# Performance work log

Hardware: AMD Instinct MI355X
Metric: run time of the kernel (lower is better)

The kernel has to match this reference:

```python
import jax, jax.numpy as jnp
import numpy as np

# Finite-difference stencils along a given axis with one-sided boundary handling:
#  'f' : forward diff  d[i]=(X[i+1]-X[i])/h, last voxel copies previous diff
#  'b' : backward diff d[i]=(X[i]-X[i-1])/h, first voxel copies next diff
#  'c' : central diff  d[i]=(X[i+1]-X[i-1])/(2h), one-sided at boundaries

def _g(X, axis, h, kind):
    Xm = jnp.moveaxis(X, axis, 0)
    d = (Xm[1:] - Xm[:-1]) / h  # length n-1 one-step diffs
    if kind == 'f':
        r = jnp.concatenate([d, d[-1:]], axis=0)
    elif kind == 'b':
        r = jnp.concatenate([d[:1], d], axis=0)
    else:  # central
        r = jnp.concatenate([d[:1], (Xm[2:] - Xm[:-2]) / (2.0 * h), d[-1:]], axis=0)
    return jnp.moveaxis(r, 0, axis)

HX = HY = HZ = 1.0  # data_spacing = [1,1,1]

dXc = lambda X: _g(X, 1, HX, 'c')
dYc = lambda X: _g(X, 2, HY, 'c')
dZc = lambda X: _g(X, 3, HZ, 'c')
dXf = lambda X: _g(X, 1, HX, 'f')
dYf = lambda X: _g(X, 2, HY, 'f')
dZf = lambda X: _g(X, 3, HZ, 'f')
dXb = lambda X: _g(X, 1, HX, 'b')
dYb = lambda X: _g(X, 2, HY, 'b')
dZb = lambda X: _g(X, 3, HZ, 'b')


def setup_inputs() -> dict:
    key = jax.random.key(0)
    ks = jax.random.split(key, 10)
    shp = (2, 160, 160, 160)
    f32 = jnp.float32
    return {
        'C':   jax.random.normal(ks[0], shp, f32),
        'Vx':  jax.random.normal(ks[1], shp, f32),
        'Vy':  jax.random.normal(ks[2], shp, f32),
        'Vz':  jax.random.normal(ks[3], shp, f32),
        'Dxx': jax.random.uniform(ks[4], shp, f32),
        'Dxy': jax.random.normal(ks[5], shp, f32) * 0.1,
        'Dxz': jax.random.normal(ks[6], shp, f32) * 0.1,
        'Dyy': jax.random.uniform(ks[7], shp, f32),
        'Dyz': jax.random.normal(ks[8], shp, f32) * 0.1,
        'Dzz': jax.random.uniform(ks[9], shp, f32),
    }


def reference(C, Vx, Vy, Vz, Dxx, Dxy, Dxz, Dyy, Dyz, Dzz):
    # --- diffusion term: Grad_fullD (3D, full symmetric tensor D) ---
    Cx_c, Cy_c, Cz_c = dXc(C), dYc(C), dZc(C)        # central grads of C
    Cx_f, Cy_f, Cz_f = dXf(C), dYf(C), dZf(C)        # forward grads of C
    diff = ((dXc(Dxx) + dYc(Dxy) + dZc(Dxz)) * Cx_c
            + (dXc(Dxy) + dYc(Dyy) + dZc(Dyz)) * Cy_c
            + (dXc(Dxz) + dYc(Dyz) + dZc(Dzz)) * Cz_c
            + Dxx * dXb(Cx_f) + Dyy * dYb(Cy_f) + Dzz * dZb(Cz_f)
            + Dxy * (dXb(Cy_f) + dYb(Cx_f))
            + Dyz * (dYb(Cz_f) + dZb(Cy_f))
            + Dxz * (dZb(Cx_f) + dXb(Cz_f)))
    # --- advection term: Grad_vectorV (upwind per-voxel on sign of V) ---
    C_x = jnp.where(Vx > 0, dXb(C), dXf(C))
    C_y = jnp.where(Vy > 0, dYb(C), dYf(C))
    C_z = jnp.where(Vz > 0, dZb(C), dZf(C))
    adv = -(Vx * C_x + Vy * C_y + Vz * C_z) - C * (dXc(Vx) + dYc(Vy) + dZc(Vz))
    return diff + adv
```

## Files before the change

### kernel.cpp

```cpp
#include <hip/hip_runtime.h>

#define N   160
#define SX  (N * N)
#define SY  N

__global__ __launch_bounds__(640) void piano_energy_kernel(
    const float* __restrict__ C,   const float* __restrict__ Vx,
    const float* __restrict__ Vy,  const float* __restrict__ Vz,
    const float* __restrict__ Dxx, const float* __restrict__ Dxy,
    const float* __restrict__ Dxz, const float* __restrict__ Dyy,
    const float* __restrict__ Dyz, const float* __restrict__ Dzz,
    float* __restrict__ out)
{
    const int z = threadIdx.x;
    const int y = blockIdx.x * 4 + threadIdx.y;
    const int x = blockIdx.y;
    const int b = blockIdx.z;

    const int idx = ((b * N + x) * N + y) * N + z;

    const bool xlo = (x > 0), xhi = (x < N - 1);
    const bool ylo = (y > 0), yhi = (y < N - 1);
    const bool zlo = (z > 0), zhi = (z < N - 1);

    const int oxp = xhi ?  SX : 0,  oxm = xlo ? -SX : 0;
    const int oyp = yhi ?  SY : 0,  oym = ylo ? -SY : 0;
    const int ozp = zhi ?   1 : 0,  ozm = zlo ?  -1 : 0;

    const float sx = (xlo && xhi) ? 0.5f : 1.f;
    const float sy = (ylo && yhi) ? 0.5f : 1.f;
    const float sz = (zlo && zhi) ? 0.5f : 1.f;

    const float c0  = C[idx];
    const float cxp = C[idx + oxp], cxm = C[idx + oxm];
    const float cyp = C[idx + oyp], cym = C[idx + oym];
    const float czp = C[idx + ozp], czm = C[idx + ozm];

    const float Cx_c = sx * (cxp - cxm);
    const float Cy_c = sy * (cyp - cym);
    const float Cz_c = sz * (czp - czm);
    const float Cx_f = xhi ? (cxp - c0) : (c0 - cxm);
    const float Cy_f = yhi ? (cyp - c0) : (c0 - cym);
    const float Cz_f = zhi ? (czp - c0) : (c0 - czm);
    const float Cx_b = xlo ? (c0 - cxm) : (cxp - c0);
    const float Cy_b = ylo ? (c0 - cym) : (cyp - c0);
    const float Cz_b = zlo ? (c0 - czm) : (czp - c0);

    float sXX, sYY, sZZ;
    if (!xhi)      sXX = 0.f;
    else if (xlo)  sXX = cxp - 2.f * c0 + cxm;
    else           sXX = C[idx + 2 * SX] - 2.f * cxp + c0;
    if (!yhi)      sYY = 0.f;
    else if (ylo)  sYY = cyp - 2.f * c0 + cym;
    else           sYY = C[idx + 2 * SY] - 2.f * cyp + c0;
    if (!zhi)      sZZ = 0.f;
    else if (zlo)  sZZ = czp - 2.f * c0 + czm;
    else           sZZ = C[idx + 2] - 2.f * czp + c0;

    const int obx1 = xlo ? 0 : SX,  obx0 = obx1 - SX;
    const int oby1 = ylo ? 0 : SY,  oby0 = oby1 - SY;
    const int obz1 = zlo ? 0 : 1,   obz0 = obz1 - 1;
    const int ofx0 = xhi ? 0 : -SX;
    const int ofy0 = yhi ? 0 : -SY;
    const int ofz0 = zhi ? 0 : -1;

    float cXY;
    if (xlo && xhi && ylo && yhi) {
        cXY = cxp + cxm + cyp + cym - 2.f * c0
            - C[idx - SX + SY] - C[idx + SX - SY];
    } else {
        cXY = (C[idx + obx1 + oyp] - C[idx + obx1 + ofy0])
            - (C[idx + obx0 + oyp] - C[idx + obx0 + ofy0])
            + (C[idx + oby1 + oxp] - C[idx + oby1 + ofx0])
            - (C[idx + oby0 + oxp] - C[idx + oby0 + ofx0]);
    }

    float cXZ;
    if (xlo && xhi && zlo && zhi) {
        cXZ = cxp + cxm + czp + czm - 2.f * c0
            - C[idx + SX - 1] - C[idx - SX + 1];
    } else {
        cXZ = (C[idx + obz1 + oxp] - C[idx + obz1 + ofx0])
            - (C[idx + obz0 + oxp] - C[idx + obz0 + ofx0])
            + (C[idx + obx1 + ozp] - C[idx + obx1 + ofz0])
            - (C[idx + obx0 + ozp] - C[idx + obx0 + ofz0]);
    }

    float cYZ;
    if (ylo && yhi && zlo && zhi) {
        cYZ = cyp + cym + czp + czm - 2.f * c0
            - C[idx + SY - 1] - C[idx - SY + 1];
    } else {
        cYZ = (C[idx + obz1 + oyp] - C[idx + obz1 + ofy0])
            - (C[idx + obz0 + oyp] - C[idx + obz0 + ofy0])
            + (C[idx + oby1 + ozp] - C[idx + oby1 + ofz0])
            - (C[idx + oby0 + ozp] - C[idx + oby0 + ofz0]);
    }

    const float dDxx_x = sx * (Dxx[idx + oxp] - Dxx[idx + oxm]);
    const float dDxy_x = sx * (Dxy[idx + oxp] - Dxy[idx + oxm]);
    const float dDxy_y = sy * (Dxy[idx + oyp] - Dxy[idx + oym]);
    const float dDxz_x = sx * (Dxz[idx + oxp] - Dxz[idx + oxm]);
    const float dDxz_z = sz * (Dxz[idx + ozp] - Dxz[idx + ozm]);
    const float dDyy_y = sy * (Dyy[idx + oyp] - Dyy[idx + oym]);
    const float dDyz_y = sy * (Dyz[idx + oyp] - Dyz[idx + oym]);
    const float dDyz_z = sz * (Dyz[idx + ozp] - Dyz[idx + ozm]);
    const float dDzz_z = sz * (Dzz[idx + ozp] - Dzz[idx + ozm]);

    const float t1 = dDxx_x + dDxy_y + dDxz_z;
    const float t2 = dDxy_x + dDyy_y + dDyz_z;
    const float t3 = dDxz_x + dDyz_y + dDzz_z;

    const float Dxx0 = Dxx[idx], Dyy0 = Dyy[idx], Dzz0 = Dzz[idx];
    const float Dxy0 = Dxy[idx], Dyz0 = Dyz[idx], Dxz0 = Dxz[idx];

    const float diff = t1 * Cx_c + t2 * Cy_c + t3 * Cz_c
                     + Dxx0 * sXX + Dyy0 * sYY + Dzz0 * sZZ
                     + Dxy0 * cXY + Dyz0 * cYZ + Dxz0 * cXZ;

    const float Vx0 = Vx[idx], Vy0 = Vy[idx], Vz0 = Vz[idx];
    const float dVx = sx * (Vx[idx + oxp] - Vx[idx + oxm]);
    const float dVy = sy * (Vy[idx + oyp] - Vy[idx + oym]);
    const float dVz = sz * (Vz[idx + ozp] - Vz[idx + ozm]);

    const float C_x = (Vx0 > 0.f) ? Cx_b : Cx_f;
    const float C_y = (Vy0 > 0.f) ? Cy_b : Cy_f;
    const float C_z = (Vz0 > 0.f) ? Cz_b : Cz_f;

    const float adv = -(Vx0 * C_x + Vy0 * C_y + Vz0 * C_z)
                    - c0 * (dVx + dVy + dVz);

    out[idx] = diff + adv;
}

extern "C" void kernel_launch(void* const* d_in, const int* in_sizes, int n_in,
                              void* d_out, int out_size, void* d_ws, size_t ws_size,
                              hipStream_t stream) {
    const float* C   = (const float*)d_in[0];
    const float* Vx  = (const float*)d_in[1];
    const float* Vy  = (const float*)d_in[2];
    const float* Vz  = (const float*)d_in[3];
    const float* Dxx = (const float*)d_in[4];
    const float* Dxy = (const float*)d_in[5];
    const float* Dxz = (const float*)d_in[6];
    const float* Dyy = (const float*)d_in[7];
    const float* Dyz = (const float*)d_in[8];
    const float* Dzz = (const float*)d_in[9];
    float* out = (float*)d_out;

    dim3 grid(N / 4, N, 2);
    dim3 block(N, 4, 1);
    hipLaunchKernelGGL(piano_energy_kernel, grid, block, 0, stream,
                       C, Vx, Vy, Vz, Dxx, Dxy, Dxz, Dyy, Dyz, Dzz, out);
}
```

Measured before the change: 357.6 us.

## Vectorize stencil to four z-points per thread with float4 loads and swizzled block mapping

Each thread now computes four consecutive z voxels, loading neighbour rows as float4 and reusing them in registers for the z-direction stencils. This cuts redundant per-voxel scalar loads and per-element address arithmetic. The grid is flattened with a block-index swizzle that interleaves x slices, meant to improve L2 locality across concurrently running blocks. Launch bounds change to 320 threads with a minimum occupancy hint. Register pressure rises, and the boundary paths still fall back to scalar gathers.

```diff
diff --git a/kernel.cpp b/kernel.cpp
--- a/kernel.cpp
+++ b/kernel.cpp
@@ -4,7 +4,27 @@
 #define SX  (N * N)
 #define SY  N
 
-__global__ __launch_bounds__(640) void piano_energy_kernel(
+
+struct R4 { float a[4]; };
+struct R6 { float a[6]; };
+
+__device__ __forceinline__ R4 ld4(const float* __restrict__ p, int row, int z0) {
+    const float4 m = *reinterpret_cast<const float4*>(p + row * N + z0);
+    R4 r; r.a[0] = m.x; r.a[1] = m.y; r.a[2] = m.z; r.a[3] = m.w;
+    return r;
+}
+
+__device__ __forceinline__ R6 ld6(const float* __restrict__ p, int row, int z0,
+                                  int zL, int zR) {
+    const float4 m = *reinterpret_cast<const float4*>(p + row * N + z0);
+    R6 r;
+    r.a[0] = p[row * N + z0 + zL];
+    r.a[1] = m.x; r.a[2] = m.y; r.a[3] = m.z; r.a[4] = m.w;
+    r.a[5] = p[row * N + z0 + zR];
+    return r;
+}
+
+__global__ __launch_bounds__(320, 4) void piano_energy_kernel(
     const float* __restrict__ C,   const float* __restrict__ Vx,
     const float* __restrict__ Vy,  const float* __restrict__ Vz,
     const float* __restrict__ Dxx, const float* __restrict__ Dxy,
@@ -12,125 +32,250 @@
     const float* __restrict__ Dyz, const float* __restrict__ Dzz,
     float* __restrict__ out)
 {
-    const int z = threadIdx.x;
-    const int y = blockIdx.x * 4 + threadIdx.y;
-    const int x = blockIdx.y;
-    const int b = blockIdx.z;
-
-    const int idx = ((b * N + x) * N + y) * N + z;
+    const int tz = threadIdx.x;
+    const int z0 = tz << 2;
+
+    const int id = blockIdx.x;
+    const int w  = (id & 7) * 800 + (id >> 3);
+    const int x  = w % N;
+    const int g  = w / N;
+    const int y  = (g % 20) * 8 + threadIdx.y;
+    const int b  = g / 20;
+
+    const int r0  = (b * N + x) * N + y;
+    const int idx = r0 * N + z0;
 
     const bool xlo = (x > 0), xhi = (x < N - 1);
     const bool ylo = (y > 0), yhi = (y < N - 1);
-    const bool zlo = (z > 0), zhi = (z < N - 1);
-
-    const int oxp = xhi ?  SX : 0,  oxm = xlo ? -SX : 0;
-    const int oyp = yhi ?  SY : 0,  oym = ylo ? -SY : 0;
-    const int ozp = zhi ?   1 : 0,  ozm = zlo ?  -1 : 0;
+    const bool zlo0 = (tz > 0), zhi3 = (tz < 39);
+
+    const int oxp_r = xhi ?  N : 0, oxm_r = xlo ? -N : 0;
+    const int oyp_r = yhi ?  1 : 0, oym_r = ylo ? -1 : 0;
+    const int zL = zlo0 ? -1 : 0;
+    const int zR = zhi3 ?  4 : 3;
 
     const float sx = (xlo && xhi) ? 0.5f : 1.f;
     const float sy = (ylo && yhi) ? 0.5f : 1.f;
-    const float sz = (zlo && zhi) ? 0.5f : 1.f;
-
-    const float c0  = C[idx];
-    const float cxp = C[idx + oxp], cxm = C[idx + oxm];
-    const float cyp = C[idx + oyp], cym = C[idx + oym];
-    const float czp = C[idx + ozp], czm = C[idx + ozm];
-
-    const float Cx_c = sx * (cxp - cxm);
-    const float Cy_c = sy * (cyp - cym);
-    const float Cz_c = sz * (czp - czm);
-    const float Cx_f = xhi ? (cxp - c0) : (c0 - cxm);
-    const float Cy_f = yhi ? (cyp - c0) : (c0 - cym);
-    const float Cz_f = zhi ? (czp - c0) : (c0 - czm);
-    const float Cx_b = xlo ? (c0 - cxm) : (cxp - c0);
-    const float Cy_b = ylo ? (c0 - cym) : (cyp - c0);
-    const float Cz_b = zlo ? (c0 - czm) : (czp - c0);
-
-    float sXX, sYY, sZZ;
-    if (!xhi)      sXX = 0.f;
-    else if (xlo)  sXX = cxp - 2.f * c0 + cxm;
-    else           sXX = C[idx + 2 * SX] - 2.f * cxp + c0;
-    if (!yhi)      sYY = 0.f;
-    else if (ylo)  sYY = cyp - 2.f * c0 + cym;
-    else           sYY = C[idx + 2 * SY] - 2.f * cyp + c0;
-    if (!zhi)      sZZ = 0.f;
-    else if (zlo)  sZZ = czp - 2.f * c0 + czm;
-    else           sZZ = C[idx + 2] - 2.f * czp + c0;
-
-    const int obx1 = xlo ? 0 : SX,  obx0 = obx1 - SX;
-    const int oby1 = ylo ? 0 : SY,  oby0 = oby1 - SY;
-    const int obz1 = zlo ? 0 : 1,   obz0 = obz1 - 1;
-    const int ofx0 = xhi ? 0 : -SX;
-    const int ofy0 = yhi ? 0 : -SY;
-    const int ofz0 = zhi ? 0 : -1;
-
-    float cXY;
-    if (xlo && xhi && ylo && yhi) {
-        cXY = cxp + cxm + cyp + cym - 2.f * c0
-            - C[idx - SX + SY] - C[idx + SX - SY];
-    } else {
-        cXY = (C[idx + obx1 + oyp] - C[idx + obx1 + ofy0])
-            - (C[idx + obx0 + oyp] - C[idx + obx0 + ofy0])
-            + (C[idx + oby1 + oxp] - C[idx + oby1 + ofx0])
-            - (C[idx + oby0 + oxp] - C[idx + oby0 + ofx0]);
-    }
-
-    float cXZ;
-    if (xlo && xhi && zlo && zhi) {
-        cXZ = cxp + cxm + czp + czm - 2.f * c0
-            - C[idx + SX - 1] - C[idx - SX + 1];
-    } else {
-        cXZ = (C[idx + obz1 + oxp] - C[idx + obz1 + ofx0])
-            - (C[idx + obz0 + oxp] - C[idx + obz0 + ofx0])
-            + (C[idx + obx1 + ozp] - C[idx + obx1 + ofz0])
-            - (C[idx + obx0 + ozp] - C[idx + obx0 + ofz0]);
-    }
-
-    float cYZ;
-    if (ylo && yhi && zlo && zhi) {
-        cYZ = cyp + cym + czp + czm - 2.f * c0
-            - C[idx + SY - 1] - C[idx - SY + 1];
-    } else {
-        cYZ = (C[idx + obz1 + oyp] - C[idx + obz1 + ofy0])
-            - (C[idx + obz0 + oyp] - C[idx + obz0 + ofy0])
-            + (C[idx + oby1 + ozp] - C[idx + oby1 + ofz0])
-            - (C[idx + oby0 + ozp] - C[idx + oby0 + ofz0]);
-    }
-
-    const float dDxx_x = sx * (Dxx[idx + oxp] - Dxx[idx + oxm]);
-    const float dDxy_x = sx * (Dxy[idx + oxp] - Dxy[idx + oxm]);
-    const float dDxy_y = sy * (Dxy[idx + oyp] - Dxy[idx + oym]);
-    const float dDxz_x = sx * (Dxz[idx + oxp] - Dxz[idx + oxm]);
-    const float dDxz_z = sz * (Dxz[idx + ozp] - Dxz[idx + ozm]);
-    const float dDyy_y = sy * (Dyy[idx + oyp] - Dyy[idx + oym]);
-    const float dDyz_y = sy * (Dyz[idx + oyp] - Dyz[idx + oym]);
-    const float dDyz_z = sz * (Dyz[idx + ozp] - Dyz[idx + ozm]);
-    const float dDzz_z = sz * (Dzz[idx + ozp] - Dzz[idx + ozm]);
-
-    const float t1 = dDxx_x + dDxy_y + dDxz_z;
-    const float t2 = dDxy_x + dDyy_y + dDyz_z;
-    const float t3 = dDxz_x + dDyz_y + dDzz_z;
-
-    const float Dxx0 = Dxx[idx], Dyy0 = Dyy[idx], Dzz0 = Dzz[idx];
-    const float Dxy0 = Dxy[idx], Dyz0 = Dyz[idx], Dxz0 = Dxz[idx];
-
-    const float diff = t1 * Cx_c + t2 * Cy_c + t3 * Cz_c
-                     + Dxx0 * sXX + Dyy0 * sYY + Dzz0 * sZZ
-                     + Dxy0 * cXY + Dyz0 * cYZ + Dxz0 * cXZ;
-
-    const float Vx0 = Vx[idx], Vy0 = Vy[idx], Vz0 = Vz[idx];
-    const float dVx = sx * (Vx[idx + oxp] - Vx[idx + oxm]);
-    const float dVy = sy * (Vy[idx + oyp] - Vy[idx + oym]);
-    const float dVz = sz * (Vz[idx + ozp] - Vz[idx + ozm]);
-
-    const float C_x = (Vx0 > 0.f) ? Cx_b : Cx_f;
-    const float C_y = (Vy0 > 0.f) ? Cy_b : Cy_f;
-    const float C_z = (Vz0 > 0.f) ? Cz_b : Cz_f;
-
-    const float adv = -(Vx0 * C_x + Vy0 * C_y + Vz0 * C_z)
-                    - c0 * (dVx + dVy + dVz);
-
-    out[idx] = diff + adv;
+
+    const int oxp = xhi ? SX : 0, ofx0 = xhi ? 0 : -SX;
+    const int oyp = yhi ? SY : 0, ofy0 = yhi ? 0 : -SY;
+    const int obx1 = xlo ? 0 : SX, obx0 = obx1 - SX;
+    const int oby1 = ylo ? 0 : SY, oby0 = oby1 - SY;
+
+    const R6 Cc  = ld6(C, r0,         z0, zL, zR);
+    const R6 Cxp = ld6(C, r0 + oxp_r, z0, zL, zR);
+    const R6 Cxm = ld6(C, r0 + oxm_r, z0, zL, zR);
+    const R6 Cyp = ld6(C, r0 + oyp_r, z0, zL, zR);
+    const R6 Cym = ld6(C, r0 + oym_r, z0, zL, zR);
+    const R4 Ca  = ld4(C, r0 + oxm_r + oyp_r, z0);
+    const R4 Cb  = ld4(C, r0 + oxp_r + oym_r, z0);
+
+    R4 Cx2 = {}; R4 Cy2 = {};
+    if (!xlo && xhi) Cx2 = ld4(C, r0 + 2 * N, z0);
+    if (!ylo && yhi) Cy2 = ld4(C, r0 + 2, z0);
+
+    float Cxc[4], Cyc[4], Czc[4];
+    float sXXa[4], sYYa[4], sZZa[4], cXYa[4], cXZa[4], cYZa[4];
+
+#pragma unroll
+    for (int e = 0; e < 4; ++e) {
+        const bool zlo = (e > 0) || zlo0;
+        const bool zhi = (e < 3) || zhi3;
+        const float sz = (zlo && zhi) ? 0.5f : 1.f;
+        const float c0  = Cc.a[e + 1];
+        const float cxp = Cxp.a[e + 1], cxm = Cxm.a[e + 1];
+        const float cyp = Cyp.a[e + 1], cym = Cym.a[e + 1];
+        const float czp = zhi ? Cc.a[e + 2] : c0;
+        const float czm = zlo ? Cc.a[e]     : c0;
+
+        Cxc[e] = sx * (cxp - cxm);
+        Cyc[e] = sy * (cyp - cym);
+        Czc[e] = sz * (czp - czm);
+
+        float sXX, sYY, sZZ;
+        if (!xhi)      sXX = 0.f;
+        else if (xlo)  sXX = cxp - 2.f * c0 + cxm;
+        else           sXX = Cx2.a[e] - 2.f * cxp + c0;
+        if (!yhi)      sYY = 0.f;
+        else if (ylo)  sYY = cyp - 2.f * c0 + cym;
+        else           sYY = Cy2.a[e] - 2.f * cyp + c0;
+        if (!zhi)      sZZ = 0.f;
+        else if (zlo)  sZZ = czp - 2.f * c0 + czm;
+        else           sZZ = Cc.a[(e + 3 > 5) ? 5 : e + 3] - 2.f * czp + c0;
+        sXXa[e] = sXX; sYYa[e] = sYY; sZZa[e] = sZZ;
+
+        const int gi = idx + e;
+        if (xlo && xhi && ylo && yhi) {
+            cXYa[e] = cxp + cxm + cyp + cym - 2.f * c0 - Ca.a[e] - Cb.a[e];
+        } else {
+            cXYa[e] = (C[gi + obx1 + oyp] - C[gi + obx1 + ofy0])
+                    - (C[gi + obx0 + oyp] - C[gi + obx0 + ofy0])
+                    + (C[gi + oby1 + oxp] - C[gi + oby1 + ofx0])
+                    - (C[gi + oby0 + oxp] - C[gi + oby0 + ofx0]);
+        }
+        if (xlo && xhi && zlo && zhi) {
+            cXZa[e] = cxp + cxm + czp + czm - 2.f * c0
+                    - Cxp.a[e] - Cxm.a[e + 2];
+        } else {
+            const int ozp = zhi ? 1 : 0;
+            const int obz1 = zlo ? 0 : 1, obz0 = obz1 - 1;
+            const int ofz0 = zhi ? 0 : -1;
+            cXZa[e] = (C[gi + obz1 + oxp] - C[gi + obz1 + ofx0])
+                    - (C[gi + obz0 + oxp] - C[gi + obz0 + ofx0])
+                    + (C[gi + obx1 + ozp] - C[gi + obx1 + ofz0])
+                    - (C[gi + obx0 + ozp] - C[gi + obx0 + ofz0]);
+        }
+        if (ylo && yhi && zlo && zhi) {
+            cYZa[e] = cyp + cym + czp + czm - 2.f * c0
+                    - Cyp.a[e] - Cym.a[e + 2];
+        } else {
+            const int ozp = zhi ? 1 : 0;
+            const int obz1 = zlo ? 0 : 1, obz0 = obz1 - 1;
+            const int ofz0 = zhi ? 0 : -1;
+            cYZa[e] = (C[gi + obz1 + oyp] - C[gi + obz1 + ofy0])
+                    - (C[gi + obz0 + oyp] - C[gi + obz0 + ofy0])
+                    + (C[gi + oby1 + ozp] - C[gi + oby1 + ofz0])
+                    - (C[gi + oby0 + ozp] - C[gi + oby0 + ofz0]);
+        }
+    }
+
+    float t1a[4], t2a[4], t3a[4], acc[4];
+
+    {
+        const R4 c = ld4(Dxx, r0, z0);
+        const R4 p = ld4(Dxx, r0 + oxp_r, z0);
+        const R4 m = ld4(Dxx, r0 + oxm_r, z0);
+#pragma unroll
+        for (int e = 0; e < 4; ++e) {
+            t1a[e] = sx * (p.a[e] - m.a[e]);
+            acc[e] = c.a[e] * sXXa[e];
+        }
+    }
+    {
+        const R4 c  = ld4(Dxy, r0, z0);
+        const R4 xp = ld4(Dxy, r0 + oxp_r, z0);
+        const R4 xm = ld4(Dxy, r0 + oxm_r, z0);
+        const R4 yp = ld4(Dxy, r0 + oyp_r, z0);
+        const R4 ym = ld4(Dxy, r0 + oym_r, z0);
+#pragma unroll
+        for (int e = 0; e < 4; ++e) {
+            t1a[e] += sy * (yp.a[e] - ym.a[e]);
+            t2a[e]  = sx * (xp.a[e] - xm.a[e]);
+            acc[e] += c.a[e] * cXYa[e];
+        }
+    }
+    {
+        const R6 c  = ld6(Dxz, r0, z0, zL, zR);
+        const R4 xp = ld4(Dxz, r0 + oxp_r, z0);
+        const R4 xm = ld4(Dxz, r0 + oxm_r, z0);
+#pragma unroll
+        for (int e = 0; e < 4; ++e) {
+            const bool zlo = (e > 0) || zlo0;
+            const bool zhi = (e < 3) || zhi3;
+            const float sz = (zlo && zhi) ? 0.5f : 1.f;
+            const float zpv = zhi ? c.a[e + 2] : c.a[e + 1];
+            const float zmv = zlo ? c.a[e]     : c.a[e + 1];
+            t1a[e] += sz * (zpv - zmv);
+            t3a[e]  = sx * (xp.a[e] - xm.a[e]);
+            acc[e] += c.a[e + 1] * cXZa[e];
+        }
+    }
+    {
+        const R4 c  = ld4(Dyy, r0, z0);
+        const R4 yp = ld4(Dyy, r0 + oyp_r, z0);
+        const R4 ym = ld4(Dyy, r0 + oym_r, z0);
+#pragma unroll
+        for (int e = 0; e < 4; ++e) {
+            t2a[e] += sy * (yp.a[e] - ym.a[e]);
+            acc[e] += c.a[e] * sYYa[e];
+        }
+    }
+    {
+        const R6 c  = ld6(Dyz, r0, z0, zL, zR);
+        const R4 yp = ld4(Dyz, r0 + oyp_r, z0);
+        const R4 ym = ld4(Dyz, r0 + oym_r, z0);
+#pragma unroll
+        for (int e = 0; e < 4; ++e) {
+            const bool zlo = (e > 0) || zlo0;
+            const bool zhi = (e < 3) || zhi3;
+            const float sz = (zlo && zhi) ? 0.5f : 1.f;
+            const float zpv = zhi ? c.a[e + 2] : c.a[e + 1];
+            const float zmv = zlo ? c.a[e]     : c.a[e + 1];
+            t2a[e] += sz * (zpv - zmv);
+            t3a[e] += sy * (yp.a[e] - ym.a[e]);
+            acc[e] += c.a[e + 1] * cYZa[e];
+        }
+    }
+    {
+        const R6 c = ld6(Dzz, r0, z0, zL, zR);
+#pragma unroll
+        for (int e = 0; e < 4; ++e) {
+            const bool zlo = (e > 0) || zlo0;
+            const bool zhi = (e < 3) || zhi3;
+            const float sz = (zlo && zhi) ? 0.5f : 1.f;
+            const float zpv = zhi ? c.a[e + 2] : c.a[e + 1];
+            const float zmv = zlo ? c.a[e]     : c.a[e + 1];
+            t3a[e] += sz * (zpv - zmv);
+            acc[e] += c.a[e + 1] * sZZa[e];
+        }
+    }
+
+#pragma unroll
+    for (int e = 0; e < 4; ++e)
+        acc[e] += t1a[e] * Cxc[e] + t2a[e] * Cyc[e] + t3a[e] * Czc[e];
+
+    {
+        const R4 c = ld4(Vx, r0, z0);
+        const R4 p = ld4(Vx, r0 + oxp_r, z0);
+        const R4 m = ld4(Vx, r0 + oxm_r, z0);
+#pragma unroll
+        for (int e = 0; e < 4; ++e) {
+            const float c0  = Cc.a[e + 1];
+            const float cxp = Cxp.a[e + 1], cxm = Cxm.a[e + 1];
+            const float Cx_f = xhi ? (cxp - c0) : (c0 - cxm);
+            const float Cx_b = xlo ? (c0 - cxm) : (cxp - c0);
+            const float v = c.a[e];
+            acc[e] -= v * ((v > 0.f) ? Cx_b : Cx_f)
+                    + c0 * (sx * (p.a[e] - m.a[e]));
+        }
+    }
+    {
+        const R4 c = ld4(Vy, r0, z0);
+        const R4 p = ld4(Vy, r0 + oyp_r, z0);
+        const R4 m = ld4(Vy, r0 + oym_r, z0);
+#pragma unroll
+        for (int e = 0; e < 4; ++e) {
+            const float c0  = Cc.a[e + 1];
+            const float cyp = Cyp.a[e + 1], cym = Cym.a[e + 1];
+            const float Cy_f = yhi ? (cyp - c0) : (c0 - cym);
+            const float Cy_b = ylo ? (c0 - cym) : (cyp - c0);
+            const float v = c.a[e];
+            acc[e] -= v * ((v > 0.f) ? Cy_b : Cy_f)
+                    + c0 * (sy * (p.a[e] - m.a[e]));
+        }
+    }
+    {
+        const R6 c = ld6(Vz, r0, z0, zL, zR);
+#pragma unroll
+        for (int e = 0; e < 4; ++e) {
+            const bool zlo = (e > 0) || zlo0;
+            const bool zhi = (e < 3) || zhi3;
+            const float sz = (zlo && zhi) ? 0.5f : 1.f;
+            const float c0  = Cc.a[e + 1];
+            const float czp = zhi ? Cc.a[e + 2] : c0;
+            const float czm = zlo ? Cc.a[e]     : c0;
+            const float Cz_f = zhi ? (czp - c0) : (c0 - czm);
+            const float Cz_b = zlo ? (c0 - czm) : (czp - c0);
+            const float v = c.a[e + 1];
+            const float dVz = sz * ((zhi ? c.a[e + 2] : c.a[e + 1])
+                                  - (zlo ? c.a[e]     : c.a[e + 1]));
+            acc[e] -= v * ((v > 0.f) ? Cz_b : Cz_f) + c0 * dVz;
+        }
+    }
+
+    float4 o;
+    o.x = acc[0]; o.y = acc[1]; o.z = acc[2]; o.w = acc[3];
+    *reinterpret_cast<float4*>(out + idx) = o;
 }
 
 extern "C" void kernel_launch(void* const* d_in, const int* in_sizes, int n_in,
@@ -148,8 +293,8 @@
     const float* Dzz = (const float*)d_in[9];
     float* out = (float*)d_out;
 
-    dim3 grid(N / 4, N, 2);
-    dim3 block(N, 4, 1);
+    dim3 grid(6400, 1, 1);
+    dim3 block(40, 8, 1);
     hipLaunchKernelGGL(piano_energy_kernel, grid, block, 0, stream,
                        C, Vx, Vy, Vz, Dxx, Dxy, Dxz, Dyy, Dyz, Dzz, out);
 }
```

New measurement: 716.7 us. 100% more time.

## Stage stencil input tiles into LDS and swizzle block ordering

Applied to the files above, without the earlier changes.

Each block cooperatively loads the needed x-planes and y-halo rows of all ten input fields into shared memory with vectorized float4 loads, then computes the stencil from LDS. The grid is flattened and block indices are swizzled so neighbouring work is spread across the device. This aims to cut redundant global/cache reads of neighbour values, at the cost of large LDS use per block (lower occupancy) and extra reloading of x-neighbour planes across blocks.

```diff
diff --git a/kernel.cpp b/kernel.cpp
--- a/kernel.cpp
+++ b/kernel.cpp
@@ -1,10 +1,31 @@
 #include <hip/hip_runtime.h>
 
-#define N   160
-#define SX  (N * N)
-#define SY  N
-
-__global__ __launch_bounds__(640) void piano_energy_kernel(
+#define N    160
+#define SX   (N * N)
+#define SY   N
+#define ROW  160
+
+
+template<int P, int R, bool HALO>
+__device__ __forceinline__ void stage(float* __restrict__ lds, int dstRow,
+                                      const float* __restrict__ src,
+                                      int b, int x, int y0, int tid)
+{
+    const int tot = P * R * 40;
+    for (int u = tid; u < tot; u += 640) {
+        const int c = u % 40;
+        const int r = (u / 40) % R;
+        const int p = u / (40 * R);
+        const int px = (P == 3) ? min(max(x + p - 1, 0), N - 1) : x;
+        int gy = HALO ? (y0 + r - 1) : (y0 + r);
+        if (HALO) gy = min(max(gy, 0), N - 1);
+        const float4 v = *reinterpret_cast<const float4*>(
+            src + ((b * N + px) * N + gy) * N + (c << 2));
+        *reinterpret_cast<float4*>(lds + (dstRow + p * R + r) * ROW + (c << 2)) = v;
+    }
+}
+
+__global__ __launch_bounds__(640, 2) void piano_energy_kernel(
     const float* __restrict__ C,   const float* __restrict__ Vx,
     const float* __restrict__ Vy,  const float* __restrict__ Vz,
     const float* __restrict__ Dxx, const float* __restrict__ Dxy,
@@ -12,10 +33,32 @@
     const float* __restrict__ Dyz, const float* __restrict__ Dzz,
     float* __restrict__ out)
 {
-    const int z = threadIdx.x;
-    const int y = blockIdx.x * 4 + threadIdx.y;
-    const int x = blockIdx.y;
-    const int b = blockIdx.z;
+    __shared__ float lds[98 * ROW];
+
+    const int id = blockIdx.x;
+    const int w  = (id & 7) * 1600 + (id >> 3);
+    const int x  = w % N;
+    const int g  = w / N;
+    const int y0 = (g % 40) * 4;
+    const int b  = g / 40;
+
+    const int z   = threadIdx.x;
+    const int ty  = threadIdx.y;
+    const int tid = ty * 160 + z;
+    const int y   = y0 + ty;
+    const int jc  = ty + 1;
+
+    stage<3, 6, true >(lds,  0, C,   b, x, y0, tid);
+    stage<3, 4, false>(lds, 18, Dxx, b, x, y0, tid);
+    stage<3, 6, true >(lds, 30, Dxy, b, x, y0, tid);
+    stage<3, 4, false>(lds, 48, Dxz, b, x, y0, tid);
+    stage<3, 4, false>(lds, 60, Vx,  b, x, y0, tid);
+    stage<1, 6, true >(lds, 72, Dyy, b, x, y0, tid);
+    stage<1, 6, true >(lds, 78, Dyz, b, x, y0, tid);
+    stage<1, 6, true >(lds, 84, Vy,  b, x, y0, tid);
+    stage<1, 4, false>(lds, 90, Dzz, b, x, y0, tid);
+    stage<1, 4, false>(lds, 94, Vz,  b, x, y0, tid);
+    __syncthreads();
 
     const int idx = ((b * N + x) * N + y) * N + z;
 
@@ -23,18 +66,29 @@
     const bool ylo = (y > 0), yhi = (y < N - 1);
     const bool zlo = (z > 0), zhi = (z < N - 1);
 
-    const int oxp = xhi ?  SX : 0,  oxm = xlo ? -SX : 0;
-    const int oyp = yhi ?  SY : 0,  oym = ylo ? -SY : 0;
-    const int ozp = zhi ?   1 : 0,  ozm = zlo ?  -1 : 0;
+    const int xp = 1 + (xhi ? 1 : 0), xm = 1 - (xlo ? 1 : 0);
+    const int yp = jc + (yhi ? 1 : 0), ym = jc - (ylo ? 1 : 0);
+    const int zp = z + (zhi ? 1 : 0),  zm = z - (zlo ? 1 : 0);
 
     const float sx = (xlo && xhi) ? 0.5f : 1.f;
     const float sy = (ylo && yhi) ? 0.5f : 1.f;
     const float sz = (zlo && zhi) ? 0.5f : 1.f;
 
-    const float c0  = C[idx];
-    const float cxp = C[idx + oxp], cxm = C[idx + oxm];
-    const float cyp = C[idx + oyp], cym = C[idx + oym];
-    const float czp = C[idx + ozp], czm = C[idx + ozm];
+#define CL(p,j,zz)   lds[((p) * 6 + (j)) * ROW + (zz)]
+#define DXXL(p,zz)   lds[(18 + (p) * 4 + ty) * ROW + (zz)]
+#define DXYL(p,j,zz) lds[(30 + (p) * 6 + (j)) * ROW + (zz)]
+#define DXZL(p,zz)   lds[(48 + (p) * 4 + ty) * ROW + (zz)]
+#define VXL(p,zz)    lds[(60 + (p) * 4 + ty) * ROW + (zz)]
+#define DYYL(j,zz)   lds[(72 + (j)) * ROW + (zz)]
+#define DYZL(j,zz)   lds[(78 + (j)) * ROW + (zz)]
+#define VYL(j,zz)    lds[(84 + (j)) * ROW + (zz)]
+#define DZZL(zz)     lds[(90 + ty) * ROW + (zz)]
+#define VZL(zz)      lds[(94 + ty) * ROW + (zz)]
+
+    const float c0  = CL(1, jc, z);
+    const float cxp = CL(xp, jc, z), cxm = CL(xm, jc, z);
+    const float cyp = CL(1, yp, z),  cym = CL(1, ym, z);
+    const float czp = CL(1, jc, zp), czm = CL(1, jc, zm);
 
     const float Cx_c = sx * (cxp - cxm);
     const float Cy_c = sy * (cyp - cym);
@@ -52,76 +106,76 @@
     else           sXX = C[idx + 2 * SX] - 2.f * cxp + c0;
     if (!yhi)      sYY = 0.f;
     else if (ylo)  sYY = cyp - 2.f * c0 + cym;
-    else           sYY = C[idx + 2 * SY] - 2.f * cyp + c0;
+    else           sYY = CL(1, jc + 2, z) - 2.f * cyp + c0;
     if (!zhi)      sZZ = 0.f;
     else if (zlo)  sZZ = czp - 2.f * c0 + czm;
-    else           sZZ = C[idx + 2] - 2.f * czp + c0;
-
-    const int obx1 = xlo ? 0 : SX,  obx0 = obx1 - SX;
-    const int oby1 = ylo ? 0 : SY,  oby0 = oby1 - SY;
-    const int obz1 = zlo ? 0 : 1,   obz0 = obz1 - 1;
-    const int ofx0 = xhi ? 0 : -SX;
-    const int ofy0 = yhi ? 0 : -SY;
+    else           sZZ = CL(1, jc, 2) - 2.f * czp + c0;
+
+    const int obx1 = xlo ? 0 : 1, obx0 = obx1 - 1;
+    const int oby1 = ylo ? 0 : 1, oby0 = oby1 - 1;
+    const int obz1 = zlo ? 0 : 1, obz0 = obz1 - 1;
+    const int ofx0 = xhi ? 0 : -1;
+    const int ofy0 = yhi ? 0 : -1;
     const int ofz0 = zhi ? 0 : -1;
 
     float cXY;
     if (xlo && xhi && ylo && yhi) {
         cXY = cxp + cxm + cyp + cym - 2.f * c0
-            - C[idx - SX + SY] - C[idx + SX - SY];
+            - CL(0, jc + 1, z) - CL(2, jc - 1, z);
     } else {
-        cXY = (C[idx + obx1 + oyp] - C[idx + obx1 + ofy0])
-            - (C[idx + obx0 + oyp] - C[idx + obx0 + ofy0])
-            + (C[idx + oby1 + oxp] - C[idx + oby1 + ofx0])
-            - (C[idx + oby0 + oxp] - C[idx + oby0 + ofx0]);
+        cXY = (CL(1 + obx1, yp, z) - CL(1 + obx1, jc + ofy0, z))
+            - (CL(1 + obx0, yp, z) - CL(1 + obx0, jc + ofy0, z))
+            + (CL(xp, jc + oby1, z) - CL(1 + ofx0, jc + oby1, z))
+            - (CL(xp, jc + oby0, z) - CL(1 + ofx0, jc + oby0, z));
     }
 
     float cXZ;
     if (xlo && xhi && zlo && zhi) {
         cXZ = cxp + cxm + czp + czm - 2.f * c0
-            - C[idx + SX - 1] - C[idx - SX + 1];
+            - CL(2, jc, z - 1) - CL(0, jc, z + 1);
     } else {
-        cXZ = (C[idx + obz1 + oxp] - C[idx + obz1 + ofx0])
-            - (C[idx + obz0 + oxp] - C[idx + obz0 + ofx0])
-            + (C[idx + obx1 + ozp] - C[idx + obx1 + ofz0])
-            - (C[idx + obx0 + ozp] - C[idx + obx0 + ofz0]);
+        cXZ = (CL(xp, jc, z + obz1) - CL(1 + ofx0, jc, z + obz1))
+            - (CL(xp, jc, z + obz0) - CL(1 + ofx0, jc, z + obz0))
+            + (CL(1 + obx1, jc, zp) - CL(1 + obx1, jc, z + ofz0))
+            - (CL(1 + obx0, jc, zp) - CL(1 + obx0, jc, z + ofz0));
     }
 
     float cYZ;
     if (ylo && yhi && zlo && zhi) {
         cYZ = cyp + cym + czp + czm - 2.f * c0
-            - C[idx + SY - 1] - C[idx - SY + 1];
+            - CL(1, jc + 1, z - 1) - CL(1, jc - 1, z + 1);
     } else {
-        cYZ = (C[idx + obz1 + oyp] - C[idx + obz1 + ofy0])
-            - (C[idx + obz0 + oyp] - C[idx + obz0 + ofy0])
-            + (C[idx + oby1 + ozp] - C[idx + oby1 + ofz0])
-            - (C[idx + oby0 + ozp] - C[idx + oby0 + ofz0]);
-    }
-
-    const float dDxx_x = sx * (Dxx[idx + oxp] - Dxx[idx + oxm]);
-    const float dDxy_x = sx * (Dxy[idx + oxp] - Dxy[idx + oxm]);
-    const float dDxy_y = sy * (Dxy[idx + oyp] - Dxy[idx + oym]);
-    const float dDxz_x = sx * (Dxz[idx + oxp] - Dxz[idx + oxm]);
-    const float dDxz_z = sz * (Dxz[idx + ozp] - Dxz[idx + ozm]);
-    const float dDyy_y = sy * (Dyy[idx + oyp] - Dyy[idx + oym]);
-    const float dDyz_y = sy * (Dyz[idx + oyp] - Dyz[idx + oym]);
-    const float dDyz_z = sz * (Dyz[idx + ozp] - Dyz[idx + ozm]);
-    const float dDzz_z = sz * (Dzz[idx + ozp] - Dzz[idx + ozm]);
+        cYZ = (CL(1, yp, z + obz1) - CL(1, jc + ofy0, z + obz1))
+            - (CL(1, yp, z + obz0) - CL(1, jc + ofy0, z + obz0))
+            + (CL(1, jc + oby1, zp) - CL(1, jc + oby1, z + ofz0))
+            - (CL(1, jc + oby0, zp) - CL(1, jc + oby0, z + ofz0));
+    }
+
+    const float dDxx_x = sx * (DXXL(xp, z) - DXXL(xm, z));
+    const float dDxy_x = sx * (DXYL(xp, jc, z) - DXYL(xm, jc, z));
+    const float dDxy_y = sy * (DXYL(1, yp, z) - DXYL(1, ym, z));
+    const float dDxz_x = sx * (DXZL(xp, z) - DXZL(xm, z));
+    const float dDxz_z = sz * (DXZL(1, zp) - DXZL(1, zm));
+    const float dDyy_y = sy * (DYYL(yp, z) - DYYL(ym, z));
+    const float dDyz_y = sy * (DYZL(yp, z) - DYZL(ym, z));
+    const float dDyz_z = sz * (DYZL(jc, zp) - DYZL(jc, zm));
+    const float dDzz_z = sz * (DZZL(zp) - DZZL(zm));
 
     const float t1 = dDxx_x + dDxy_y + dDxz_z;
     const float t2 = dDxy_x + dDyy_y + dDyz_z;
     const float t3 = dDxz_x + dDyz_y + dDzz_z;
 
-    const float Dxx0 = Dxx[idx], Dyy0 = Dyy[idx], Dzz0 = Dzz[idx];
-    const float Dxy0 = Dxy[idx], Dyz0 = Dyz[idx], Dxz0 = Dxz[idx];
+    const float Dxx0 = DXXL(1, z), Dyy0 = DYYL(jc, z), Dzz0 = DZZL(z);
+    const float Dxy0 = DXYL(1, jc, z), Dyz0 = DYZL(jc, z), Dxz0 = DXZL(1, z);
 
     const float diff = t1 * Cx_c + t2 * Cy_c + t3 * Cz_c
                      + Dxx0 * sXX + Dyy0 * sYY + Dzz0 * sZZ
                      + Dxy0 * cXY + Dyz0 * cYZ + Dxz0 * cXZ;
 
-    const float Vx0 = Vx[idx], Vy0 = Vy[idx], Vz0 = Vz[idx];
-    const float dVx = sx * (Vx[idx + oxp] - Vx[idx + oxm]);
-    const float dVy = sy * (Vy[idx + oyp] - Vy[idx + oym]);
-    const float dVz = sz * (Vz[idx + ozp] - Vz[idx + ozm]);
+    const float Vx0 = VXL(1, z), Vy0 = VYL(jc, z), Vz0 = VZL(z);
+    const float dVx = sx * (VXL(xp, z) - VXL(xm, z));
+    const float dVy = sy * (VYL(yp, z) - VYL(ym, z));
+    const float dVz = sz * (VZL(zp) - VZL(zm));
 
     const float C_x = (Vx0 > 0.f) ? Cx_b : Cx_f;
     const float C_y = (Vy0 > 0.f) ? Cy_b : Cy_f;
@@ -148,8 +202,8 @@
     const float* Dzz = (const float*)d_in[9];
     float* out = (float*)d_out;
 
-    dim3 grid(N / 4, N, 2);
-    dim3 block(N, 4, 1);
+    dim3 grid(12800, 1, 1);
+    dim3 block(160, 4, 1);
     hipLaunchKernelGGL(piano_energy_kernel, grid, block, 0, stream,
                        C, Vx, Vy, Vz, Dxx, Dxy, Dxz, Dyy, Dyz, Dzz, out);
 }
```

Result: slower. 519.1 us (+45.1%).

## Process two z-voxels per thread with float2 vector loads and stores

Applied to the files above, without the earlier changes.

Each thread now computes two adjacent z outputs, using float2 loads for the center and x/y neighbours. The z-neighbour values come from the pair itself, so only the two outer halo values need scalar loads. This is meant to cut the load instruction count and the redundant z-neighbour fetches. Block size is halved to 320 threads with a min-blocks hint of 4, and the boundary and cross-derivative logic had to be rewritten by hand for the two lanes, which risks edge-case errors.

```diff
diff --git a/kernel.cpp b/kernel.cpp
--- a/kernel.cpp
+++ b/kernel.cpp
@@ -4,7 +4,18 @@
 #define SX  (N * N)
 #define SY  N
 
-__global__ __launch_bounds__(640) void piano_energy_kernel(
+
+__device__ __forceinline__ float crossG(const float* __restrict__ P, int gi,
+                                        int op1, int of1, int ob1a, int ob1b,
+                                        int op2, int of2, int ob2a, int ob2b)
+{
+    return (P[gi + ob1a + op1] - P[gi + ob1a + of1])
+         - (P[gi + ob1b + op1] - P[gi + ob1b + of1])
+         + (P[gi + ob2a + op2] - P[gi + ob2a + of2])
+         - (P[gi + ob2b + op2] - P[gi + ob2b + of2]);
+}
+
+__global__ __launch_bounds__(320, 4) void piano_energy_kernel(
     const float* __restrict__ C,   const float* __restrict__ Vx,
     const float* __restrict__ Vy,  const float* __restrict__ Vz,
     const float* __restrict__ Dxx, const float* __restrict__ Dxy,
@@ -12,125 +23,174 @@
     const float* __restrict__ Dyz, const float* __restrict__ Dzz,
     float* __restrict__ out)
 {
-    const int z = threadIdx.x;
-    const int y = blockIdx.x * 4 + threadIdx.y;
-    const int x = blockIdx.y;
-    const int b = blockIdx.z;
-
-    const int idx = ((b * N + x) * N + y) * N + z;
+    const int z0 = threadIdx.x << 1;
+    const int y  = blockIdx.x * 4 + threadIdx.y;
+    const int x  = blockIdx.y;
+    const int b  = blockIdx.z;
+
+    const int idx0 = ((b * N + x) * N + y) * N + z0;
 
     const bool xlo = (x > 0), xhi = (x < N - 1);
     const bool ylo = (y > 0), yhi = (y < N - 1);
-    const bool zlo = (z > 0), zhi = (z < N - 1);
-
-    const int oxp = xhi ?  SX : 0,  oxm = xlo ? -SX : 0;
-    const int oyp = yhi ?  SY : 0,  oym = ylo ? -SY : 0;
-    const int ozp = zhi ?   1 : 0,  ozm = zlo ?  -1 : 0;
-
-    const float sx = (xlo && xhi) ? 0.5f : 1.f;
-    const float sy = (ylo && yhi) ? 0.5f : 1.f;
-    const float sz = (zlo && zhi) ? 0.5f : 1.f;
-
-    const float c0  = C[idx];
-    const float cxp = C[idx + oxp], cxm = C[idx + oxm];
-    const float cyp = C[idx + oyp], cym = C[idx + oym];
-    const float czp = C[idx + ozp], czm = C[idx + ozm];
-
-    const float Cx_c = sx * (cxp - cxm);
-    const float Cy_c = sy * (cyp - cym);
-    const float Cz_c = sz * (czp - czm);
-    const float Cx_f = xhi ? (cxp - c0) : (c0 - cxm);
-    const float Cy_f = yhi ? (cyp - c0) : (c0 - cym);
-    const float Cz_f = zhi ? (czp - c0) : (c0 - czm);
-    const float Cx_b = xlo ? (c0 - cxm) : (cxp - c0);
-    const float Cy_b = ylo ? (c0 - cym) : (cyp - c0);
-    const float Cz_b = zlo ? (c0 - czm) : (czp - c0);
-
-    float sXX, sYY, sZZ;
-    if (!xhi)      sXX = 0.f;
-    else if (xlo)  sXX = cxp - 2.f * c0 + cxm;
-    else           sXX = C[idx + 2 * SX] - 2.f * cxp + c0;
-    if (!yhi)      sYY = 0.f;
-    else if (ylo)  sYY = cyp - 2.f * c0 + cym;
-    else           sYY = C[idx + 2 * SY] - 2.f * cyp + c0;
-    if (!zhi)      sZZ = 0.f;
-    else if (zlo)  sZZ = czp - 2.f * c0 + czm;
-    else           sZZ = C[idx + 2] - 2.f * czp + c0;
-
-    const int obx1 = xlo ? 0 : SX,  obx0 = obx1 - SX;
-    const int oby1 = ylo ? 0 : SY,  oby0 = oby1 - SY;
-    const int obz1 = zlo ? 0 : 1,   obz0 = obz1 - 1;
+    const bool zloA = (z0 > 0);
+    const bool zhiB = (z0 + 1 < N - 1);
+
+    const int oxp = xhi ?  SX : 0, oxm = xlo ? -SX : 0;
+    const int oyp = yhi ?  SY : 0, oym = ylo ? -SY : 0;
+    const int ozmA = zloA ? -1 : 0;
+    const int ozpB = zhiB ?  2 : 1;
+
+    const float sx  = (xlo && xhi) ? 0.5f : 1.f;
+    const float sy  = (ylo && yhi) ? 0.5f : 1.f;
+    const float szA = zloA ? 0.5f : 1.f;
+    const float szB = zhiB ? 0.5f : 1.f;
+
+#define F2(P, off) (*reinterpret_cast<const float2*>((P) + idx0 + (off)))
+
+    const float2 cc  = F2(C, 0);
+    const float2 cxp = F2(C, oxp), cxm = F2(C, oxm);
+    const float2 cyp = F2(C, oyp), cym = F2(C, oym);
+    const float2 cab = F2(C, oxm + oyp);
+    const float2 cba = F2(C, oxp + oym);
+    const float czmA    = C[idx0 + ozmA];
+    const float czpB    = C[idx0 + ozpB];
+    const float cxp_zm  = C[idx0 + oxp + ozmA];
+    const float cxm_zp2 = C[idx0 + oxm + ozpB];
+    const float cyp_zm  = C[idx0 + oyp + ozmA];
+    const float cym_zp2 = C[idx0 + oym + ozpB];
+    float2 cx2 = make_float2(0.f, 0.f), cy2 = make_float2(0.f, 0.f);
+    if (!xlo && xhi) cx2 = F2(C, 2 * SX);
+    if (!ylo && yhi) cy2 = F2(C, 2 * SY);
+
+    const float cA = cc.x, cB = cc.y;
+
+    const float CxcA = sx * (cxp.x - cxm.x), CxcB = sx * (cxp.y - cxm.y);
+    const float CycA = sy * (cyp.x - cym.x), CycB = sy * (cyp.y - cym.y);
+    const float CzcA = szA * (cB - czmA),    CzcB = szB * (czpB - cA);
+
+    const float CxfA = xhi ? (cxp.x - cA) : (cA - cxm.x);
+    const float CxfB = xhi ? (cxp.y - cB) : (cB - cxm.y);
+    const float CyfA = yhi ? (cyp.x - cA) : (cA - cym.x);
+    const float CyfB = yhi ? (cyp.y - cB) : (cB - cym.y);
+    const float CzfA = cB - cA;
+    const float CzfB = zhiB ? (czpB - cB) : (cB - cA);
+
+    const float CxbA = xlo ? (cA - cxm.x) : (cxp.x - cA);
+    const float CxbB = xlo ? (cB - cxm.y) : (cxp.y - cB);
+    const float CybA = ylo ? (cA - cym.x) : (cyp.x - cA);
+    const float CybB = ylo ? (cB - cym.y) : (cyp.y - cB);
+    const float CzbA = zloA ? (cA - czmA) : (cB - cA);
+    const float CzbB = cB - cA;
+
+    float sXXA, sXXB, sYYA, sYYB, sZZA, sZZB;
+    if (!xhi)      { sXXA = 0.f;                          sXXB = 0.f; }
+    else if (xlo)  { sXXA = cxp.x - 2.f * cA + cxm.x;     sXXB = cxp.y - 2.f * cB + cxm.y; }
+    else           { sXXA = cx2.x - 2.f * cxp.x + cA;     sXXB = cx2.y - 2.f * cxp.y + cB; }
+    if (!yhi)      { sYYA = 0.f;                          sYYB = 0.f; }
+    else if (ylo)  { sYYA = cyp.x - 2.f * cA + cym.x;     sYYB = cyp.y - 2.f * cB + cym.y; }
+    else           { sYYA = cy2.x - 2.f * cyp.x + cA;     sYYB = cy2.y - 2.f * cyp.y + cB; }
+    sZZA = zloA ? (cB - 2.f * cA + czmA) : (czpB - 2.f * cB + cA);
+    sZZB = zhiB ? (czpB - 2.f * cB + cA) : 0.f;
+
     const int ofx0 = xhi ? 0 : -SX;
     const int ofy0 = yhi ? 0 : -SY;
-    const int ofz0 = zhi ? 0 : -1;
-
-    float cXY;
+    const int obx1 = xlo ? 0 : SX, obx0 = obx1 - SX;
+    const int oby1 = ylo ? 0 : SY, oby0 = oby1 - SY;
+
+    float cXYA, cXYB;
     if (xlo && xhi && ylo && yhi) {
-        cXY = cxp + cxm + cyp + cym - 2.f * c0
-            - C[idx - SX + SY] - C[idx + SX - SY];
-    } else {
-        cXY = (C[idx + obx1 + oyp] - C[idx + obx1 + ofy0])
-            - (C[idx + obx0 + oyp] - C[idx + obx0 + ofy0])
-            + (C[idx + oby1 + oxp] - C[idx + oby1 + ofx0])
-            - (C[idx + oby0 + oxp] - C[idx + oby0 + ofx0]);
-    }
-
-    float cXZ;
-    if (xlo && xhi && zlo && zhi) {
-        cXZ = cxp + cxm + czp + czm - 2.f * c0
-            - C[idx + SX - 1] - C[idx - SX + 1];
-    } else {
-        cXZ = (C[idx + obz1 + oxp] - C[idx + obz1 + ofx0])
-            - (C[idx + obz0 + oxp] - C[idx + obz0 + ofx0])
-            + (C[idx + obx1 + ozp] - C[idx + obx1 + ofz0])
-            - (C[idx + obx0 + ozp] - C[idx + obx0 + ofz0]);
-    }
-
-    float cYZ;
-    if (ylo && yhi && zlo && zhi) {
-        cYZ = cyp + cym + czp + czm - 2.f * c0
-            - C[idx + SY - 1] - C[idx - SY + 1];
-    } else {
-        cYZ = (C[idx + obz1 + oyp] - C[idx + obz1 + ofy0])
-            - (C[idx + obz0 + oyp] - C[idx + obz0 + ofy0])
-            + (C[idx + oby1 + ozp] - C[idx + oby1 + ofz0])
-            - (C[idx + oby0 + ozp] - C[idx + oby0 + ofz0]);
-    }
-
-    const float dDxx_x = sx * (Dxx[idx + oxp] - Dxx[idx + oxm]);
-    const float dDxy_x = sx * (Dxy[idx + oxp] - Dxy[idx + oxm]);
-    const float dDxy_y = sy * (Dxy[idx + oyp] - Dxy[idx + oym]);
-    const float dDxz_x = sx * (Dxz[idx + oxp] - Dxz[idx + oxm]);
-    const float dDxz_z = sz * (Dxz[idx + ozp] - Dxz[idx + ozm]);
-    const float dDyy_y = sy * (Dyy[idx + oyp] - Dyy[idx + oym]);
-    const float dDyz_y = sy * (Dyz[idx + oyp] - Dyz[idx + oym]);
-    const float dDyz_z = sz * (Dyz[idx + ozp] - Dyz[idx + ozm]);
-    const float dDzz_z = sz * (Dzz[idx + ozp] - Dzz[idx + ozm]);
-
-    const float t1 = dDxx_x + dDxy_y + dDxz_z;
-    const float t2 = dDxy_x + dDyy_y + dDyz_z;
-    const float t3 = dDxz_x + dDyz_y + dDzz_z;
-
-    const float Dxx0 = Dxx[idx], Dyy0 = Dyy[idx], Dzz0 = Dzz[idx];
-    const float Dxy0 = Dxy[idx], Dyz0 = Dyz[idx], Dxz0 = Dxz[idx];
-
-    const float diff = t1 * Cx_c + t2 * Cy_c + t3 * Cz_c
-                     + Dxx0 * sXX + Dyy0 * sYY + Dzz0 * sZZ
-                     + Dxy0 * cXY + Dyz0 * cYZ + Dxz0 * cXZ;
-
-    const float Vx0 = Vx[idx], Vy0 = Vy[idx], Vz0 = Vz[idx];
-    const float dVx = sx * (Vx[idx + oxp] - Vx[idx + oxm]);
-    const float dVy = sy * (Vy[idx + oyp] - Vy[idx + oym]);
-    const float dVz = sz * (Vz[idx + ozp] - Vz[idx + ozm]);
-
-    const float C_x = (Vx0 > 0.f) ? Cx_b : Cx_f;
-    const float C_y = (Vy0 > 0.f) ? Cy_b : Cy_f;
-    const float C_z = (Vz0 > 0.f) ? Cz_b : Cz_f;
-
-    const float adv = -(Vx0 * C_x + Vy0 * C_y + Vz0 * C_z)
-                    - c0 * (dVx + dVy + dVz);
-
-    out[idx] = diff + adv;
+        cXYA = cxp.x + cxm.x + cyp.x + cym.x - 2.f * cA - cab.x - cba.x;
+        cXYB = cxp.y + cxm.y + cyp.y + cym.y - 2.f * cB - cab.y - cba.y;
+    } else {
+        cXYA = crossG(C, idx0,     oyp, ofy0, obx1, obx0, oxp, ofx0, oby1, oby0);
+        cXYB = crossG(C, idx0 + 1, oyp, ofy0, obx1, obx0, oxp, ofx0, oby1, oby0);
+    }
+
+    float cXZA, cXZB;
+    if (xlo && xhi && zloA) {
+        cXZA = cxp.x + cxm.x + cB + czmA - 2.f * cA - cxp_zm - cxm.y;
+    } else {
+        const int obz1 = zloA ? 0 : 1, obz0 = obz1 - 1;
+        cXZA = crossG(C, idx0, oxp, ofx0, obz1, obz0, 1, 0, obx1, obx0);
+    }
+    if (xlo && xhi && zhiB) {
+        cXZB = cxp.y + cxm.y + czpB + cA - 2.f * cB - cxp.x - cxm_zp2;
+    } else {
+        const int ozp = zhiB ? 1 : 0, ofz0 = zhiB ? 0 : -1;
+        cXZB = crossG(C, idx0 + 1, oxp, ofx0, 0, -1, ozp, ofz0, obx1, obx0);
+    }
+
+    float cYZA, cYZB;
+    if (ylo && yhi && zloA) {
+        cYZA = cyp.x + cym.x + cB + czmA - 2.f * cA - cyp_zm - cym.y;
+    } else {
+        const int obz1 = zloA ? 0 : 1, obz0 = obz1 - 1;
+        cYZA = crossG(C, idx0, oyp, ofy0, obz1, obz0, 1, 0, oby1, oby0);
+    }
+    if (ylo && yhi && zhiB) {
+        cYZB = cyp.y + cym.y + czpB + cA - 2.f * cB - cyp.x - cym_zp2;
+    } else {
+        const int ozp = zhiB ? 1 : 0, ofz0 = zhiB ? 0 : -1;
+        cYZB = crossG(C, idx0 + 1, oyp, ofy0, 0, -1, ozp, ofz0, oby1, oby0);
+    }
+
+    float t1A, t2A, t3A, accA, t1B, t2B, t3B, accB;
+    {
+        const float2 dc = F2(Dxx, 0), dp = F2(Dxx, oxp), dm = F2(Dxx, oxm);
+        t1A = sx * (dp.x - dm.x);  accA = dc.x * sXXA;
+        t1B = sx * (dp.y - dm.y);  accB = dc.y * sXXB;
+    }
+    {
+        const float2 dc = F2(Dxy, 0), dxp2 = F2(Dxy, oxp), dxm2 = F2(Dxy, oxm);
+        const float2 dyp2 = F2(Dxy, oyp), dym2 = F2(Dxy, oym);
+        t1A += sy * (dyp2.x - dym2.x);  t2A = sx * (dxp2.x - dxm2.x);  accA += dc.x * cXYA;
+        t1B += sy * (dyp2.y - dym2.y);  t2B = sx * (dxp2.y - dxm2.y);  accB += dc.y * cXYB;
+    }
+    {
+        const float2 dc = F2(Dxz, 0), dp = F2(Dxz, oxp), dm = F2(Dxz, oxm);
+        const float dzm = Dxz[idx0 + ozmA], dzp = Dxz[idx0 + ozpB];
+        t1A += szA * (dc.y - dzm);  t3A = sx * (dp.x - dm.x);  accA += dc.x * cXZA;
+        t1B += szB * (dzp - dc.x);  t3B = sx * (dp.y - dm.y);  accB += dc.y * cXZB;
+    }
+    {
+        const float2 dc = F2(Dyy, 0), dp = F2(Dyy, oyp), dm = F2(Dyy, oym);
+        t2A += sy * (dp.x - dm.x);  accA += dc.x * sYYA;
+        t2B += sy * (dp.y - dm.y);  accB += dc.y * sYYB;
+    }
+    {
+        const float2 dc = F2(Dyz, 0), dp = F2(Dyz, oyp), dm = F2(Dyz, oym);
+        const float dzm = Dyz[idx0 + ozmA], dzp = Dyz[idx0 + ozpB];
+        t2A += szA * (dc.y - dzm);  t3A += sy * (dp.x - dm.x);  accA += dc.x * cYZA;
+        t2B += szB * (dzp - dc.x);  t3B += sy * (dp.y - dm.y);  accB += dc.y * cYZB;
+    }
+    {
+        const float2 dc = F2(Dzz, 0);
+        const float dzm = Dzz[idx0 + ozmA], dzp = Dzz[idx0 + ozpB];
+        t3A += szA * (dc.y - dzm);  accA += dc.x * sZZA;
+        t3B += szB * (dzp - dc.x);  accB += dc.y * sZZB;
+    }
+    accA += t1A * CxcA + t2A * CycA + t3A * CzcA;
+    accB += t1B * CxcB + t2B * CycB + t3B * CzcB;
+
+    {
+        const float2 vc = F2(Vx, 0), vp = F2(Vx, oxp), vm = F2(Vx, oxm);
+        accA -= vc.x * ((vc.x > 0.f) ? CxbA : CxfA) + cA * (sx * (vp.x - vm.x));
+        accB -= vc.y * ((vc.y > 0.f) ? CxbB : CxfB) + cB * (sx * (vp.y - vm.y));
+    }
+    {
+        const float2 vc = F2(Vy, 0), vp = F2(Vy, oyp), vm = F2(Vy, oym);
+        accA -= vc.x * ((vc.x > 0.f) ? CybA : CyfA) + cA * (sy * (vp.x - vm.x));
+        accB -= vc.y * ((vc.y > 0.f) ? CybB : CyfB) + cB * (sy * (vp.y - vm.y));
+    }
+    {
+        const float2 vc = F2(Vz, 0);
+        const float vzm = Vz[idx0 + ozmA], vzp = Vz[idx0 + ozpB];
+        accA -= vc.x * ((vc.x > 0.f) ? CzbA : CzfA) + cA * (szA * (vc.y - vzm));
+        accB -= vc.y * ((vc.y > 0.f) ? CzbB : CzfB) + cB * (szB * (vzp - vc.x));
+    }
+
+    *reinterpret_cast<float2*>(out + idx0) = make_float2(accA, accB);
+#undef F2
 }
 
 extern "C" void kernel_launch(void* const* d_in, const int* in_sizes, int n_in,
@@ -149,7 +209,7 @@
     float* out = (float*)d_out;
 
     dim3 grid(N / 4, N, 2);
-    dim3 block(N, 4, 1);
+    dim3 block(N / 2, 4, 1);
     hipLaunchKernelGGL(piano_energy_kernel, grid, block, 0, stream,
                        C, Vx, Vy, Vz, Dxx, Dxy, Dxz, Dyy, Dyz, Dzz, out);
 }
```

Result: slower. 374.5 us (+4.7%).
